# Kernel optimization log

Hardware: AMD Instinct MI355X
Metric: run time of the kernel (lower is better)

## Reference

```python
import jax, jax.numpy as jnp
import numpy as np

B, C, NA = 32, 9, 65440
GAMMA = 3.0
SCALE_XY = 1.0 / 0.1
SCALE_WH = 1.0 / 0.2


def setup_inputs() -> dict:
    key = jax.random.key(0)
    k1, k2, k3, k4, k5 = jax.random.split(key, 5)
    bbox_delta = jax.random.normal(k1, (B, 4, NA), dtype=jnp.float32)
    confs = jax.random.normal(k2, (B, C, NA), dtype=jnp.float32)
    # gt boxes in xywh, keep w/h strictly positive for the log() in _loc_vec
    gt_bbox = jax.random.uniform(k3, (B, NA, 4), dtype=jnp.float32, minval=0.05, maxval=1.0)
    gt_labels = jax.random.randint(k4, (B, NA), 0, C, dtype=jnp.int32)
    anchors = jax.random.uniform(k5, (1, 4, NA), dtype=jnp.float32, minval=0.1, maxval=1.0)
    return {"bbox_delta": bbox_delta, "confs": confs, "gt_bbox": gt_bbox,
            "gt_labels": gt_labels, "anchors": anchors}


def reference(bbox_delta, confs, gt_bbox, gt_labels, anchors):
    n_classes = confs.shape[1]
    # ---- focal classification loss (fused: no one-hot materialized) ----
    # alpha = [10, 1000, ..., 1000]; einsum 'a,bcd->bad' followed by sum(dim=1)
    # collapses to multiplying by sum(alpha) since y is one-hot over c.
    alpha = jnp.full((n_classes,), 1000.0, dtype=jnp.float32).at[0].set(10.0)
    logp = jax.nn.log_softmax(confs, axis=1)              # [B,C,N]
    t = gt_labels.astype(jnp.int32)[:, None, :]           # [B,1,N]
    logp_t = jnp.take_along_axis(logp, t, axis=1)[:, 0, :]  # [B,N]
    p_t = jnp.exp(logp_t)
    focal = (1.0 - p_t) ** GAMMA * logp_t                 # [B,N]
    classification_loss = jnp.mean(-jnp.sum(alpha) * focal)

    # ---- localization loss (masked smooth-L1, no boolean compaction) ----
    gt_t = jnp.transpose(gt_bbox, (0, 2, 1))               # [B,4,N]
    gxy = SCALE_XY * (gt_t[:, :2, :] - anchors[:, :2, :]) / anchors[:, 2:, :]
    gwh = SCALE_WH * jnp.log(gt_t[:, 2:, :] / anchors[:, 2:, :])
    gt_loc = jnp.concatenate([gxy, gwh], axis=1)           # [B,4,N]

    pos = gt_labels > 0                                    # [B,N]
    mask = pos[:, None, :]                                 # broadcast over 4 coords
    diff = jnp.where(mask, bbox_delta - gt_loc, 0.0)
    ad = jnp.abs(diff)
    sl1 = jnp.where(ad < 1.0, 0.5 * diff * diff, ad - 0.5)
    regression_loss = jnp.sum(jnp.where(mask, sl1, 0.0))
    num_pos = jnp.sum(pos).astype(jnp.float32)

    total_loss = regression_loss / num_pos + classification_loss
    return total_loss
```

## Files before the change

### kernel.cpp

```cpp
#include <hip/hip_runtime.h>
#include <math.h>

constexpr int B  = 32;
constexpr int C  = 9;
constexpr int NA = 65440;
constexpr int BLOCK   = 256;
constexpr int NTH     = B * NA;
constexpr int GRID    = NTH / BLOCK;

constexpr int WS_REG = 8192;
constexpr int WS_POS = 16384;
constexpr size_t WS_NEEDED = (size_t)(WS_POS + 8192) * sizeof(float);

__device__ __forceinline__ float smooth_l1(float d) {
    float ad = fabsf(d);
    return ad < 1.0f ? 0.5f * d * d : ad - 0.5f;
}

template <bool ATOMIC>
__global__ __launch_bounds__(BLOCK, 4) void ssd_main(
    const float* __restrict__ bbox_delta,
    const float* __restrict__ confs,
    const float* __restrict__ gt_bbox,
    const int*   __restrict__ gt_labels,
    const float* __restrict__ anchors,
    float* __restrict__ ws)
{
    const int tid = blockIdx.x * BLOCK + threadIdx.x;
    const int b   = tid / NA;
    const int a   = tid - b * NA;

    const float* cb = confs + (size_t)b * C * NA + a;
    float c0 = cb[0];
    float c1 = cb[1 * NA];
    float c2 = cb[2 * NA];
    float c3 = cb[3 * NA];
    float c4 = cb[4 * NA];
    float c5 = cb[5 * NA];
    float c6 = cb[6 * NA];
    float c7 = cb[7 * NA];
    float c8 = cb[8 * NA];

    const int lab = gt_labels[(size_t)b * NA + a];

    const float ax = anchors[a];
    const float ay = anchors[NA + a];
    const float aw = anchors[2 * NA + a];
    const float ah = anchors[3 * NA + a];

    const float* db = bbox_delta + (size_t)b * 4 * NA + a;
    const float d0 = db[0];
    const float d1 = db[NA];
    const float d2 = db[2 * NA];
    const float d3 = db[3 * NA];

    const float4 g = *reinterpret_cast<const float4*>(gt_bbox + ((size_t)b * NA + a) * 4);

    float cf[C] = {c0, c1, c2, c3, c4, c5, c6, c7, c8};
    float se = 0.f;
    float ct = c0;
#pragma unroll
    for (int c = 0; c < C; ++c) {
        se += __expf(cf[c]);
        ct  = (lab == c) ? cf[c] : ct;
    }
    const float lp = ct - __logf(se);
    const float p  = __expf(lp);
    const float o  = 1.f - p;
    float focal = o * o * o * lp;

    const float gx = 10.0f * __fdividef(g.x - ax, aw);
    const float gy = 10.0f * __fdividef(g.y - ay, ah);
    const float gw = 5.0f * __logf(__fdividef(g.z, aw));
    const float gh = 5.0f * __logf(__fdividef(g.w, ah));
    const float s  = smooth_l1(d0 - gx) + smooth_l1(d1 - gy) +
                     smooth_l1(d2 - gw) + smooth_l1(d3 - gh);
    const float pos = (lab > 0) ? 1.0f : 0.0f;
    float reg  = pos * s;
    float pcnt = pos;

#pragma unroll
    for (int off = 32; off > 0; off >>= 1) {
        focal += __shfl_down(focal, off, 64);
        reg   += __shfl_down(reg,   off, 64);
        pcnt  += __shfl_down(pcnt,  off, 64);
    }
    __shared__ float sf[4], sr[4], sp[4];
    const int wid  = threadIdx.x >> 6;
    const int lane = threadIdx.x & 63;
    if (lane == 0) { sf[wid] = focal; sr[wid] = reg; sp[wid] = pcnt; }
    __syncthreads();
    if (threadIdx.x == 0) {
        const float F = sf[0] + sf[1] + sf[2] + sf[3];
        const float R = sr[0] + sr[1] + sr[2] + sr[3];
        const float P = sp[0] + sp[1] + sp[2] + sp[3];
        if (ATOMIC) {
            atomicAdd(&ws[0],  F);
            atomicAdd(&ws[32], R);
            atomicAdd(&ws[64], P);
        } else {
            ws[blockIdx.x]          = F;
            ws[WS_REG + blockIdx.x] = R;
            ws[WS_POS + blockIdx.x] = P;
        }
    }
}

__global__ void zero_ws_k(float* ws) {
    int i = threadIdx.x;
    if (i < 96) ws[i] = 0.0f;
}

__global__ void finalize_atomic_k(const float* __restrict__ ws, float* __restrict__ out) {
    const float inv_n = 1.0f / (float)((size_t)B * NA);
    out[0] = ws[32] / ws[64] - 8010.0f * ws[0] * inv_n;
}

__global__ __launch_bounds__(256) void finalize_k(const float* __restrict__ ws,
                                                  float* __restrict__ out) {
    float F = 0.f, R = 0.f, P = 0.f;
    for (int i = threadIdx.x; i < GRID; i += 256) {
        F += ws[i];
        R += ws[WS_REG + i];
        P += ws[WS_POS + i];
    }
#pragma unroll
    for (int off = 32; off > 0; off >>= 1) {
        F += __shfl_down(F, off, 64);
        R += __shfl_down(R, off, 64);
        P += __shfl_down(P, off, 64);
    }
    __shared__ float sf[4], sr[4], sp[4];
    const int wid  = threadIdx.x >> 6;
    const int lane = threadIdx.x & 63;
    if (lane == 0) { sf[wid] = F; sr[wid] = R; sp[wid] = P; }
    __syncthreads();
    if (threadIdx.x == 0) {
        const float Ft = sf[0] + sf[1] + sf[2] + sf[3];
        const float Rt = sr[0] + sr[1] + sr[2] + sr[3];
        const float Pt = sp[0] + sp[1] + sp[2] + sp[3];
        const float inv_n = 1.0f / (float)((size_t)B * NA);
        out[0] = Rt / Pt - 8010.0f * Ft * inv_n;
    }
}

extern "C" void kernel_launch(void* const* d_in, const int* in_sizes, int n_in,
                              void* d_out, int out_size, void* d_ws, size_t ws_size,
                              hipStream_t stream) {
    const float* bbox_delta = (const float*)d_in[0];
    const float* confs      = (const float*)d_in[1];
    const float* gt_bbox    = (const float*)d_in[2];
    const int*   gt_labels  = (const int*)d_in[3];
    const float* anchors    = (const float*)d_in[4];
    float* ws  = (float*)d_ws;
    float* out = (float*)d_out;

    if (ws_size >= WS_NEEDED) {
        ssd_main<false><<<GRID, BLOCK, 0, stream>>>(bbox_delta, confs, gt_bbox,
                                                    gt_labels, anchors, ws);
        finalize_k<<<1, 256, 0, stream>>>(ws, out);
    } else {
        zero_ws_k<<<1, 128, 0, stream>>>(ws);
        ssd_main<true><<<GRID, BLOCK, 0, stream>>>(bbox_delta, confs, gt_bbox,
                                                   gt_labels, anchors, ws);
        finalize_atomic_k<<<1, 1, 0, stream>>>(ws, out);
    }
}
```

Measured before the change: 178.4 us.

## Process four anchors per thread with vectorized 128-bit loads

Each thread now handles four consecutive anchors, using float4 loads for confs, labels, anchors, deltas and gt boxes. The grid shrinks fourfold and so does the number of per-block partial sums. An empty asm barrier forces all loads to be issued before any compute, and p_t is computed as exp(target)/sum instead of a second exp. The cost is higher register pressure, so launch bounds drop to 2 blocks per SM, and fewer waves are available to hide memory latency.

Result: no change. 175.9 us (-1.4%).

```diff
diff --git a/kernel.cpp b/kernel.cpp
--- a/kernel.cpp
+++ b/kernel.cpp
@@ -4,13 +4,25 @@
 constexpr int B  = 32;
 constexpr int C  = 9;
 constexpr int NA = 65440;
-constexpr int BLOCK   = 256;
-constexpr int NTH     = B * NA;
-constexpr int GRID    = NTH / BLOCK;
-
-constexpr int WS_REG = 8192;
-constexpr int WS_POS = 16384;
-constexpr size_t WS_NEEDED = (size_t)(WS_POS + 8192) * sizeof(float);
+constexpr int PER_B = NA / 4;
+constexpr int BLOCK = 256;
+constexpr int GRID  = (B * PER_B) / BLOCK;
+
+constexpr int WS_REG = 2048;
+constexpr int WS_POS = 4096;
+constexpr size_t WS_NEEDED = (size_t)(WS_POS + 2048) * sizeof(float);
+
+using f4 = __attribute__((ext_vector_type(4))) float;
+using i4 = __attribute__((ext_vector_type(4))) int;
+
+__device__ __forceinline__ f4 ld4(const float* p) {
+    return *reinterpret_cast<const f4*>(p);
+}
+
+__device__ __forceinline__ f4 exp4(f4 v) {
+    f4 r; r.x = __expf(v.x); r.y = __expf(v.y); r.z = __expf(v.z); r.w = __expf(v.w);
+    return r;
+}
 
 __device__ __forceinline__ float smooth_l1(float d) {
     float ad = fabsf(d);
@@ -18,7 +30,7 @@
 }
 
 template <bool ATOMIC>
-__global__ __launch_bounds__(BLOCK, 4) void ssd_main(
+__global__ __launch_bounds__(BLOCK, 2) void ssd_main(
     const float* __restrict__ bbox_delta,
     const float* __restrict__ confs,
     const float* __restrict__ gt_bbox,
@@ -27,57 +39,92 @@
     float* __restrict__ ws)
 {
     const int tid = blockIdx.x * BLOCK + threadIdx.x;
-    const int b   = tid / NA;
-    const int a   = tid - b * NA;
-
-    const float* cb = confs + (size_t)b * C * NA + a;
-    float c0 = cb[0];
-    float c1 = cb[1 * NA];
-    float c2 = cb[2 * NA];
-    float c3 = cb[3 * NA];
-    float c4 = cb[4 * NA];
-    float c5 = cb[5 * NA];
-    float c6 = cb[6 * NA];
-    float c7 = cb[7 * NA];
-    float c8 = cb[8 * NA];
-
-    const int lab = gt_labels[(size_t)b * NA + a];
-
-    const float ax = anchors[a];
-    const float ay = anchors[NA + a];
-    const float aw = anchors[2 * NA + a];
-    const float ah = anchors[3 * NA + a];
-
-    const float* db = bbox_delta + (size_t)b * 4 * NA + a;
-    const float d0 = db[0];
-    const float d1 = db[NA];
-    const float d2 = db[2 * NA];
-    const float d3 = db[3 * NA];
-
-    const float4 g = *reinterpret_cast<const float4*>(gt_bbox + ((size_t)b * NA + a) * 4);
-
-    float cf[C] = {c0, c1, c2, c3, c4, c5, c6, c7, c8};
-    float se = 0.f;
-    float ct = c0;
+    const int b   = tid / PER_B;
+    const int a   = (tid - b * PER_B) * 4;
+
+    const float* cbase = confs + (size_t)b * C * NA + a;
+    f4 c0 = ld4(cbase);
+    f4 c1 = ld4(cbase + 1 * NA);
+    f4 c2 = ld4(cbase + 2 * NA);
+    f4 c3 = ld4(cbase + 3 * NA);
+    f4 c4 = ld4(cbase + 4 * NA);
+    f4 c5 = ld4(cbase + 5 * NA);
+    f4 c6 = ld4(cbase + 6 * NA);
+    f4 c7 = ld4(cbase + 7 * NA);
+    f4 c8 = ld4(cbase + 8 * NA);
+
+    i4 lab = *reinterpret_cast<const i4*>(gt_labels + (size_t)b * NA + a);
+
+    const float* abase = anchors + a;
+    f4 ax = ld4(abase);
+    f4 ay = ld4(abase + NA);
+    f4 aw = ld4(abase + 2 * NA);
+    f4 ah = ld4(abase + 3 * NA);
+
+    const float* dbase = bbox_delta + (size_t)b * 4 * NA + a;
+    f4 d0 = ld4(dbase);
+    f4 d1 = ld4(dbase + NA);
+    f4 d2 = ld4(dbase + 2 * NA);
+    f4 d3 = ld4(dbase + 3 * NA);
+
+    const float* gbase = gt_bbox + ((size_t)b * NA + a) * 4;
+    f4 g0 = ld4(gbase);
+    f4 g1 = ld4(gbase + 4);
+    f4 g2 = ld4(gbase + 8);
+    f4 g3 = ld4(gbase + 12);
+
+    asm volatile(""
+        : "+v"(c0), "+v"(c1), "+v"(c2), "+v"(c3), "+v"(c4),
+          "+v"(c5), "+v"(c6), "+v"(c7), "+v"(c8),
+          "+v"(ax), "+v"(ay), "+v"(aw), "+v"(ah),
+          "+v"(d0), "+v"(d1), "+v"(d2), "+v"(d3),
+          "+v"(g0), "+v"(g1), "+v"(g2), "+v"(g3),
+          "+v"(lab));
+
+    f4 cf[C] = {c0, c1, c2, c3, c4, c5, c6, c7, c8};
+    f4 se = {0.f, 0.f, 0.f, 0.f};
+    f4 ct = c0;
+    f4 pe = {0.f, 0.f, 0.f, 0.f};
 #pragma unroll
     for (int c = 0; c < C; ++c) {
-        se += __expf(cf[c]);
-        ct  = (lab == c) ? cf[c] : ct;
-    }
-    const float lp = ct - __logf(se);
-    const float p  = __expf(lp);
-    const float o  = 1.f - p;
-    float focal = o * o * o * lp;
-
-    const float gx = 10.0f * __fdividef(g.x - ax, aw);
-    const float gy = 10.0f * __fdividef(g.y - ay, ah);
-    const float gw = 5.0f * __logf(__fdividef(g.z, aw));
-    const float gh = 5.0f * __logf(__fdividef(g.w, ah));
-    const float s  = smooth_l1(d0 - gx) + smooth_l1(d1 - gy) +
-                     smooth_l1(d2 - gw) + smooth_l1(d3 - gh);
-    const float pos = (lab > 0) ? 1.0f : 0.0f;
-    float reg  = pos * s;
-    float pcnt = pos;
+        f4 e = exp4(cf[c]);
+        se += e;
+        ct.x = (lab.x == c) ? cf[c].x : ct.x;  pe.x = (lab.x == c) ? e.x : pe.x;
+        ct.y = (lab.y == c) ? cf[c].y : ct.y;  pe.y = (lab.y == c) ? e.y : pe.y;
+        ct.z = (lab.z == c) ? cf[c].z : ct.z;  pe.z = (lab.z == c) ? e.z : pe.z;
+        ct.w = (lab.w == c) ? cf[c].w : ct.w;  pe.w = (lab.w == c) ? e.w : pe.w;
+    }
+    float focal;
+    {
+        float lpx = ct.x - __logf(se.x);
+        float lpy = ct.y - __logf(se.y);
+        float lpz = ct.z - __logf(se.z);
+        float lpw = ct.w - __logf(se.w);
+        float px = __fdividef(pe.x, se.x);
+        float py = __fdividef(pe.y, se.y);
+        float pz = __fdividef(pe.z, se.z);
+        float pw = __fdividef(pe.w, se.w);
+        float ox = 1.f - px, oy = 1.f - py, oz = 1.f - pz, ow = 1.f - pw;
+        focal = ox*ox*ox*lpx + oy*oy*oy*lpy + oz*oz*oz*lpz + ow*ow*ow*lpw;
+    }
+
+    float reg = 0.f, pcnt = 0.f;
+#define DO_ANCHOR(GT, AXC, AYC, AWC, AHC, D0C, D1C, D2C, D3C, LABC)               \
+    {                                                                             \
+        float gx = 10.0f * __fdividef(GT.x - AXC, AWC);                           \
+        float gy = 10.0f * __fdividef(GT.y - AYC, AHC);                           \
+        float gw = 5.0f * __logf(__fdividef(GT.z, AWC));                          \
+        float gh = 5.0f * __logf(__fdividef(GT.w, AHC));                          \
+        float s  = smooth_l1(D0C - gx) + smooth_l1(D1C - gy) +                    \
+                   smooth_l1(D2C - gw) + smooth_l1(D3C - gh);                     \
+        float ps = (LABC > 0) ? 1.0f : 0.0f;                                      \
+        reg += ps * s; pcnt += ps;                                                \
+    }
+    DO_ANCHOR(g0, ax.x, ay.x, aw.x, ah.x, d0.x, d1.x, d2.x, d3.x, lab.x)
+    DO_ANCHOR(g1, ax.y, ay.y, aw.y, ah.y, d0.y, d1.y, d2.y, d3.y, lab.y)
+    DO_ANCHOR(g2, ax.z, ay.z, aw.z, ah.z, d0.z, d1.z, d2.z, d3.z, lab.z)
+    DO_ANCHOR(g3, ax.w, ay.w, aw.w, ah.w, d0.w, d1.w, d2.w, d3.w, lab.w)
+#undef DO_ANCHOR
 
 #pragma unroll
     for (int off = 32; off > 0; off >>= 1) {
```

## Stage per-block inputs into LDS via async global_load_lds, two anchors per thread

Applied to the files above, without the earlier changes.

Restructures the main kernel so each block covers a 512-anchor span within a single batch row. All inputs (confs, bbox_delta, gt_bbox, anchors, labels) are bulk-copied into a 44 KB LDS buffer with 16-byte global_load_lds direct loads, then each thread handles two anchors from LDS. This aims to make global reads wide and fully coalesced, remove the per-thread index division, and reuse one exp result for p_t instead of a second exp. In exchange it uses much more LDS, lowers the occupancy hint, needs clamped tail loads with validity masking, and has no overlap between the load phase and compute within a block.

Result: no change. 176.3 us (-1.2%).

```diff
diff --git a/kernel.cpp b/kernel.cpp
--- a/kernel.cpp
+++ b/kernel.cpp
@@ -1,16 +1,28 @@
 #include <hip/hip_runtime.h>
 #include <math.h>
+#include <stdint.h>
 
 constexpr int B  = 32;
 constexpr int C  = 9;
 constexpr int NA = 65440;
-constexpr int BLOCK   = 256;
-constexpr int NTH     = B * NA;
-constexpr int GRID    = NTH / BLOCK;
-
-constexpr int WS_REG = 8192;
-constexpr int WS_POS = 16384;
-constexpr size_t WS_NEEDED = (size_t)(WS_POS + 8192) * sizeof(float);
+constexpr int BLOCK = 256;
+constexpr int SPAN  = 512;
+constexpr int BPB   = (NA + SPAN - 1) / SPAN;
+constexpr int GRID  = B * BPB;
+
+constexpr int LDS_FLOATS = 11264;
+constexpr int NCHUNK = 44;
+
+constexpr int WS_REG = 4096;
+constexpr int WS_POS = 8192;
+constexpr size_t WS_NEEDED = (size_t)(WS_POS + 4096) * sizeof(float);
+
+__device__ __forceinline__ void g2lds16(const float* g, float* l) {
+    __builtin_amdgcn_global_load_lds(
+        (const __attribute__((address_space(1))) unsigned int*)(uintptr_t)g,
+        (__attribute__((address_space(3))) unsigned int*)(uintptr_t)l,
+        16, 0, 0);
+}
 
 __device__ __forceinline__ float smooth_l1(float d) {
     float ad = fabsf(d);
@@ -18,7 +30,7 @@
 }
 
 template <bool ATOMIC>
-__global__ __launch_bounds__(BLOCK, 4) void ssd_main(
+__global__ __launch_bounds__(BLOCK, 2) void ssd_main(
     const float* __restrict__ bbox_delta,
     const float* __restrict__ confs,
     const float* __restrict__ gt_bbox,
@@ -26,58 +38,94 @@
     const float* __restrict__ anchors,
     float* __restrict__ ws)
 {
-    const int tid = blockIdx.x * BLOCK + threadIdx.x;
-    const int b   = tid / NA;
-    const int a   = tid - b * NA;
-
-    const float* cb = confs + (size_t)b * C * NA + a;
-    float c0 = cb[0];
-    float c1 = cb[1 * NA];
-    float c2 = cb[2 * NA];
-    float c3 = cb[3 * NA];
-    float c4 = cb[4 * NA];
-    float c5 = cb[5 * NA];
-    float c6 = cb[6 * NA];
-    float c7 = cb[7 * NA];
-    float c8 = cb[8 * NA];
-
-    const int lab = gt_labels[(size_t)b * NA + a];
-
-    const float ax = anchors[a];
-    const float ay = anchors[NA + a];
-    const float aw = anchors[2 * NA + a];
-    const float ah = anchors[3 * NA + a];
-
-    const float* db = bbox_delta + (size_t)b * 4 * NA + a;
-    const float d0 = db[0];
-    const float d1 = db[NA];
-    const float d2 = db[2 * NA];
-    const float d3 = db[3 * NA];
-
-    const float4 g = *reinterpret_cast<const float4*>(gt_bbox + ((size_t)b * NA + a) * 4);
-
-    float cf[C] = {c0, c1, c2, c3, c4, c5, c6, c7, c8};
-    float se = 0.f;
-    float ct = c0;
-#pragma unroll
-    for (int c = 0; c < C; ++c) {
-        se += __expf(cf[c]);
-        ct  = (lab == c) ? cf[c] : ct;
-    }
-    const float lp = ct - __logf(se);
-    const float p  = __expf(lp);
-    const float o  = 1.f - p;
-    float focal = o * o * o * lp;
-
-    const float gx = 10.0f * __fdividef(g.x - ax, aw);
-    const float gy = 10.0f * __fdividef(g.y - ay, ah);
-    const float gw = 5.0f * __logf(__fdividef(g.z, aw));
-    const float gh = 5.0f * __logf(__fdividef(g.w, ah));
-    const float s  = smooth_l1(d0 - gx) + smooth_l1(d1 - gy) +
-                     smooth_l1(d2 - gw) + smooth_l1(d3 - gh);
-    const float pos = (lab > 0) ? 1.0f : 0.0f;
-    float reg  = pos * s;
-    float pcnt = pos;
+    __shared__ float lds[LDS_FLOATS];
+    __shared__ float sf[4], sr[4], sp[4];
+
+    const int bb  = blockIdx.x >> 7;
+    const int blk = blockIdx.x & 127;
+    const int a0  = blk * SPAN;
+    const int wave = threadIdx.x >> 6;
+    const int lane = threadIdx.x & 63;
+
+#pragma unroll
+    for (int i = 0; i < 11; ++i) {
+        const int q = wave + (i << 2);
+        const float* src;
+        int ebase, lim;
+        if (q < 18) {
+            int c = q >> 1, h = q & 1;
+            src = confs; ebase = bb * C * NA + c * NA + a0 + h * 256; lim = B * C * NA;
+        } else if (q < 26) {
+            int r = q - 18; int c = r >> 1, h = r & 1;
+            src = bbox_delta; ebase = bb * 4 * NA + c * NA + a0 + h * 256; lim = B * 4 * NA;
+        } else if (q < 34) {
+            int r = q - 26;
+            src = gt_bbox; ebase = (bb * NA + a0) * 4 + r * 256; lim = B * NA * 4;
+        } else if (q < 42) {
+            int r = q - 34; int c = r >> 1, h = r & 1;
+            src = anchors; ebase = c * NA + a0 + h * 256; lim = 4 * NA;
+        } else {
+            int r = q - 42;
+            src = (const float*)gt_labels; ebase = bb * NA + a0 + r * 256; lim = B * NA;
+        }
+        int e = ebase + lane * 4;
+        e = (e > lim - 4) ? (lim - 4) : e;
+        g2lds16(src + e, &lds[q * 256 + lane * 4]);
+    }
+    __syncthreads();
+
+    const int t = threadIdx.x;
+    float focal = 0.f, reg = 0.f, pcnt = 0.f;
+
+    float2 cf2[C];
+#pragma unroll
+    for (int c = 0; c < C; ++c) cf2[c] = *(const float2*)&lds[c * 512 + 2 * t];
+    float2 dd[4];
+#pragma unroll
+    for (int c = 0; c < 4; ++c) dd[c] = *(const float2*)&lds[4608 + c * 512 + 2 * t];
+    const float4 gA = *(const float4*)&lds[6656 + (2 * t) * 4];
+    const float4 gB = *(const float4*)&lds[6656 + (2 * t + 1) * 4];
+    float2 aa[4];
+#pragma unroll
+    for (int c = 0; c < 4; ++c) aa[c] = *(const float2*)&lds[8704 + c * 512 + 2 * t];
+    const int2 lb = *(const int2*)((const int*)lds + 10752 + 2 * t);
+
+#pragma unroll
+    for (int jj = 0; jj < 2; ++jj) {
+        const bool valid = (a0 + 2 * t + jj) < NA;
+        const int lab = jj ? lb.y : lb.x;
+        float se = 0.f, ct = cf2[0].x, pe = 0.f;
+#pragma unroll
+        for (int c = 0; c < C; ++c) {
+            const float cv = jj ? cf2[c].y : cf2[c].x;
+            const float e = __expf(cv);
+            se += e;
+            if (lab == c) { ct = cv; pe = e; }
+        }
+        const float lp = ct - __logf(se);
+        const float p  = __fdividef(pe, se);
+        const float o  = 1.f - p;
+        const float v  = valid ? 1.f : 0.f;
+        focal += v * (o * o * o * lp);
+        const float4 g = jj ? gB : gA;
+        const float ax = jj ? aa[0].y : aa[0].x;
+        const float ay = jj ? aa[1].y : aa[1].x;
+        const float aw = jj ? aa[2].y : aa[2].x;
+        const float ah = jj ? aa[3].y : aa[3].x;
+        const float d0 = jj ? dd[0].y : dd[0].x;
+        const float d1 = jj ? dd[1].y : dd[1].x;
+        const float d2 = jj ? dd[2].y : dd[2].x;
+        const float d3 = jj ? dd[3].y : dd[3].x;
+        const float gx = 10.0f * __fdividef(g.x - ax, aw);
+        const float gy = 10.0f * __fdividef(g.y - ay, ah);
+        const float gw = 5.0f * __logf(__fdividef(g.z, aw));
+        const float gh = 5.0f * __logf(__fdividef(g.w, ah));
+        const float s  = smooth_l1(d0 - gx) + smooth_l1(d1 - gy) +
+                         smooth_l1(d2 - gw) + smooth_l1(d3 - gh);
+        const float ps = (valid && lab > 0) ? 1.f : 0.f;
+        reg  += ps * s;
+        pcnt += ps;
+    }
 
 #pragma unroll
     for (int off = 32; off > 0; off >>= 1) {
@@ -85,12 +133,9 @@
         reg   += __shfl_down(reg,   off, 64);
         pcnt  += __shfl_down(pcnt,  off, 64);
     }
-    __shared__ float sf[4], sr[4], sp[4];
-    const int wid  = threadIdx.x >> 6;
-    const int lane = threadIdx.x & 63;
-    if (lane == 0) { sf[wid] = focal; sr[wid] = reg; sp[wid] = pcnt; }
+    if (lane == 0) { sf[wave] = focal; sr[wave] = reg; sp[wave] = pcnt; }
     __syncthreads();
-    if (threadIdx.x == 0) {
+    if (t == 0) {
         const float F = sf[0] + sf[1] + sf[2] + sf[3];
         const float R = sr[0] + sr[1] + sr[2] + sr[3];
         const float P = sp[0] + sp[1] + sp[2] + sp[3];
```
